# Kernel tuning notes

Hardware: AMD Instinct MI355X
Metric: run time of the kernel (lower is better)

The kernel has to match this reference:

```python
import jax, jax.numpy as jnp
import numpy as np

EPS = 1e-06
N, K, O = 100000, 64, 1024


def setup_inputs() -> dict:
    key = jax.random.key(0)
    k1, k2, k3 = jax.random.split(key, 3)
    # counts: non-negative read counts per particle (scaled uniform, like count data)
    counts = jnp.floor(jax.random.uniform(k1, (N, O), dtype=jnp.float32) * 10.0)
    # otu_dist: K community profiles over O OTUs (simplex rows)
    otu_raw = jax.random.uniform(k2, (K, O), dtype=jnp.float32) + 1e-3
    otu_dist = otu_raw / otu_raw.sum(axis=-1, keepdims=True)
    # comm_dist: mixture weights over K communities (simplex)
    comm_raw = jax.random.uniform(k3, (K,), dtype=jnp.float32) + 1e-3
    comm_dist = comm_raw / comm_raw.sum()
    return {"counts": counts, "otu_dist": otu_dist, "comm_dist": comm_dist}


def reference(counts, otu_dist, comm_dist):
    # (counts[:,None,:] * log(otu_dist[None,:,:]+EPS)).sum(-1) == counts @ log(otu_dist+EPS).T
    # (N,K) per-particle per-community log-likelihood + log prior weight
    log_otu = jnp.log(otu_dist + EPS)                      # (K, O)
    logsumexpand = jnp.einsum('no,ko->nk', counts, log_otu) + jnp.log(comm_dist + EPS)[None, :]
    summand = jax.scipy.special.logsumexp(logsumexpand, axis=1)  # (N,)
    return summand.sum()
```

## Files before the change

kernel.cpp:

```cpp
#include <hip/hip_runtime.h>
#include <hip/hip_bf16.h>
#include <math.h>

#define NP 100000
#define KC 64
#define OD 1024
#define EPSF 1e-6f

#define ROWS_PER_BLOCK 128
#define NBLOCKS ((NP + ROWS_PER_BLOCK - 1) / ROWS_PER_BLOCK)

typedef __attribute__((ext_vector_type(8))) short short8;
typedef __attribute__((ext_vector_type(4))) float f32x4;

#define WS_LOGW      0
#define WS_PARTIALS  256
#define WS_BHI       8192
#define WS_BLO       (8192 + KC * OD * 2)

__device__ __forceinline__ unsigned short f32_bf16_rn(float f) {
  unsigned int u = __float_as_uint(f);
  unsigned int r = u + 0x7fffu + ((u >> 16) & 1u);
  return (unsigned short)(r >> 16);
}

__global__ void prep_kernel(const float* __restrict__ otu,
                            const float* __restrict__ comm,
                            unsigned short* __restrict__ bhi,
                            unsigned short* __restrict__ blo,
                            float* __restrict__ logw) {
  int b = blockIdx.x;
  if (b < KC) {
    const float* src = otu + b * OD;
    for (int o = threadIdx.x; o < OD; o += blockDim.x) {
      float x = logf(src[o] + EPSF);
      unsigned short h = f32_bf16_rn(x);
      float hf = __uint_as_float(((unsigned int)h) << 16);
      unsigned short l = f32_bf16_rn(x - hf);
      bhi[b * OD + o] = h;
      blo[b * OD + o] = l;
    }
  } else {
    if (threadIdx.x < KC) logw[threadIdx.x] = logf(comm[threadIdx.x] + EPSF);
  }
}

__global__ __launch_bounds__(256, 3)
void ll_kernel(const float* __restrict__ counts,
               const unsigned short* __restrict__ bhi,
               const unsigned short* __restrict__ blo,
               const float* __restrict__ logw,
               double* __restrict__ partials) {
  const int tid = threadIdx.x;
  const int wave = tid >> 6;
  const int lane = tid & 63;
  const int g = lane >> 4;
  const int c = lane & 15;
  const int rowBase = blockIdx.x * ROWS_PER_BLOCK + wave * 32;

  f32x4 acc[2][4];
#pragma unroll
  for (int i = 0; i < 2; ++i)
#pragma unroll
    for (int j = 0; j < 4; ++j)
      acc[i][j] = (f32x4){0.f, 0.f, 0.f, 0.f};

  int r0 = rowBase + c;      if (r0 >= NP) r0 = NP - 1;
  int r1 = rowBase + 16 + c; if (r1 >= NP) r1 = NP - 1;
  const float* pa0 = counts + (size_t)r0 * OD + g * 8;
  const float* pa1 = counts + (size_t)r1 * OD + g * 8;
  const unsigned short* pbh = bhi + (size_t)c * OD + g * 8;
  const unsigned short* pbl = blo + (size_t)c * OD + g * 8;

  for (int ko = 0; ko < OD; ko += 32) {
    float4 a0lo = *(const float4*)(pa0 + ko);
    float4 a0hi = *(const float4*)(pa0 + ko + 4);
    float4 a1lo = *(const float4*)(pa1 + ko);
    float4 a1hi = *(const float4*)(pa1 + ko + 4);

    short8 fbh[4], fbl[4];
#pragma unroll
    for (int ct = 0; ct < 4; ++ct) {
      fbh[ct] = *(const short8*)(pbh + (size_t)(ct * 16) * OD + ko);
      fbl[ct] = *(const short8*)(pbl + (size_t)(ct * 16) * OD + ko);
    }

    union { unsigned int u[4]; short8 v; } ua0, ua1;
    ua0.u[0] = __builtin_amdgcn_perm(__float_as_uint(a0lo.y), __float_as_uint(a0lo.x), 0x07060302u);
    ua0.u[1] = __builtin_amdgcn_perm(__float_as_uint(a0lo.w), __float_as_uint(a0lo.z), 0x07060302u);
    ua0.u[2] = __builtin_amdgcn_perm(__float_as_uint(a0hi.y), __float_as_uint(a0hi.x), 0x07060302u);
    ua0.u[3] = __builtin_amdgcn_perm(__float_as_uint(a0hi.w), __float_as_uint(a0hi.z), 0x07060302u);
    ua1.u[0] = __builtin_amdgcn_perm(__float_as_uint(a1lo.y), __float_as_uint(a1lo.x), 0x07060302u);
    ua1.u[1] = __builtin_amdgcn_perm(__float_as_uint(a1lo.w), __float_as_uint(a1lo.z), 0x07060302u);
    ua1.u[2] = __builtin_amdgcn_perm(__float_as_uint(a1hi.y), __float_as_uint(a1hi.x), 0x07060302u);
    ua1.u[3] = __builtin_amdgcn_perm(__float_as_uint(a1hi.w), __float_as_uint(a1hi.z), 0x07060302u);

#pragma unroll
    for (int ct = 0; ct < 4; ++ct) {
      acc[0][ct] = __builtin_amdgcn_mfma_f32_16x16x32_bf16(ua0.v, fbh[ct], acc[0][ct], 0, 0, 0);
      acc[1][ct] = __builtin_amdgcn_mfma_f32_16x16x32_bf16(ua1.v, fbh[ct], acc[1][ct], 0, 0, 0);
      acc[0][ct] = __builtin_amdgcn_mfma_f32_16x16x32_bf16(ua0.v, fbl[ct], acc[0][ct], 0, 0, 0);
      acc[1][ct] = __builtin_amdgcn_mfma_f32_16x16x32_bf16(ua1.v, fbl[ct], acc[1][ct], 0, 0, 0);
    }
  }

  float lw[4];
#pragma unroll
  for (int ct = 0; ct < 4; ++ct) lw[ct] = logw[ct * 16 + c];

  double lsum = 0.0;
#pragma unroll
  for (int rt = 0; rt < 2; ++rt) {
#pragma unroll
    for (int r = 0; r < 4; ++r) {
      float v0 = acc[rt][0][r] + lw[0];
      float v1 = acc[rt][1][r] + lw[1];
      float v2 = acc[rt][2][r] + lw[2];
      float v3 = acc[rt][3][r] + lw[3];
      float m = fmaxf(fmaxf(v0, v1), fmaxf(v2, v3));
      m = fmaxf(m, __shfl_xor(m, 1));
      m = fmaxf(m, __shfl_xor(m, 2));
      m = fmaxf(m, __shfl_xor(m, 4));
      m = fmaxf(m, __shfl_xor(m, 8));
      float s = __expf(v0 - m) + __expf(v1 - m) + __expf(v2 - m) + __expf(v3 - m);
      s += __shfl_xor(s, 1);
      s += __shfl_xor(s, 2);
      s += __shfl_xor(s, 4);
      s += __shfl_xor(s, 8);
      float lse = m + __logf(s);
      int row = rowBase + rt * 16 + g * 4 + r;
      if (c == 0 && row < NP) lsum += (double)lse;
    }
  }
  lsum += __shfl_xor(lsum, 16);
  lsum += __shfl_xor(lsum, 32);

  __shared__ double wpart[4];
  if (lane == 0) wpart[wave] = lsum;
  __syncthreads();
  if (tid == 0) partials[blockIdx.x] = wpart[0] + wpart[1] + wpart[2] + wpart[3];
}

__global__ void finalize_kernel(const double* __restrict__ partials,
                                float* __restrict__ out) {
  double s = 0.0;
  for (int i = threadIdx.x; i < NBLOCKS; i += 256) s += partials[i];
  s += __shfl_xor(s, 1);
  s += __shfl_xor(s, 2);
  s += __shfl_xor(s, 4);
  s += __shfl_xor(s, 8);
  s += __shfl_xor(s, 16);
  s += __shfl_xor(s, 32);
  __shared__ double sp[4];
  int w = threadIdx.x >> 6, lane = threadIdx.x & 63;
  if (lane == 0) sp[w] = s;
  __syncthreads();
  if (threadIdx.x == 0) out[0] = (float)(sp[0] + sp[1] + sp[2] + sp[3]);
}

extern "C" void kernel_launch(void* const* d_in, const int* in_sizes, int n_in,
                              void* d_out, int out_size, void* d_ws, size_t ws_size,
                              hipStream_t stream) {
  const float* counts = (const float*)d_in[0];
  const float* otu    = (const float*)d_in[1];
  const float* comm   = (const float*)d_in[2];
  float* out = (float*)d_out;
  char* ws = (char*)d_ws;

  float* logw            = (float*)(ws + WS_LOGW);
  double* partials       = (double*)(ws + WS_PARTIALS);
  unsigned short* bhi    = (unsigned short*)(ws + WS_BHI);
  unsigned short* blo    = (unsigned short*)(ws + WS_BLO);

  prep_kernel<<<KC + 1, 256, 0, stream>>>(otu, comm, bhi, blo, logw);
  ll_kernel<<<NBLOCKS, 256, 0, stream>>>(counts, bhi, blo, logw, partials);
  finalize_kernel<<<1, 256, 0, stream>>>(partials, out);
}
```

Measured before the change: 616.8 us.

## Stage B fragments in LDS with double-buffered async global-to-LDS loads

The prep kernel now writes the split bf16 log-OTU matrix in a pre-swizzled per-k-tile layout matching the MFMA fragment order. The main kernel loads each k-tile of B into a double-buffered shared-memory buffer using global_load_lds, shared by all four waves. It also prefetches the next counts tile into registers while computing the current one. Previously each wave fetched its B fragments from global memory on its own. This cuts redundant global/L2 traffic and overlaps loads with MFMA work, at the cost of a block barrier every k-step and extra LDS use that may lower occupancy.

```diff
diff --git a/kernel.cpp b/kernel.cpp
--- a/kernel.cpp
+++ b/kernel.cpp
@@ -9,14 +9,14 @@
 
 #define ROWS_PER_BLOCK 128
 #define NBLOCKS ((NP + ROWS_PER_BLOCK - 1) / ROWS_PER_BLOCK)
+#define NT 32
 
 typedef __attribute__((ext_vector_type(8))) short short8;
 typedef __attribute__((ext_vector_type(4))) float f32x4;
 
 #define WS_LOGW      0
 #define WS_PARTIALS  256
-#define WS_BHI       8192
-#define WS_BLO       (8192 + KC * OD * 2)
+#define WS_BSTAGE    8192
 
 __device__ __forceinline__ unsigned short f32_bf16_rn(float f) {
   unsigned int u = __float_as_uint(f);
@@ -24,21 +24,28 @@
   return (unsigned short)(r >> 16);
 }
 
+__device__ __forceinline__ void gll16(const void* gsrc, void* lds) {
+  __builtin_amdgcn_global_load_lds(
+      (const __attribute__((address_space(1))) unsigned int*)gsrc,
+      (__attribute__((address_space(3))) unsigned int*)lds, 16, 0, 0);
+}
+
 __global__ void prep_kernel(const float* __restrict__ otu,
                             const float* __restrict__ comm,
-                            unsigned short* __restrict__ bhi,
-                            unsigned short* __restrict__ blo,
+                            unsigned short* __restrict__ bstage,
                             float* __restrict__ logw) {
   int b = blockIdx.x;
   if (b < KC) {
-    const float* src = otu + b * OD;
-    for (int o = threadIdx.x; o < OD; o += blockDim.x) {
-      float x = logf(src[o] + EPSF);
+    int c = b & 15, ct = b >> 4;
+    for (int k = threadIdx.x; k < OD; k += blockDim.x) {
+      float x = logf(otu[b * OD + k] + EPSF);
       unsigned short h = f32_bf16_rn(x);
       float hf = __uint_as_float(((unsigned int)h) << 16);
       unsigned short l = f32_bf16_rn(x - hf);
-      bhi[b * OD + o] = h;
-      blo[b * OD + o] = l;
+      int t = k >> 5, g = (k >> 3) & 3, kk = k & 7;
+      size_t base = (size_t)t * 4096 + (size_t)ct * 512 + (size_t)(g * 16 + c) * 8 + kk;
+      bstage[base] = h;
+      bstage[base + 2048] = l;
     }
   } else {
     if (threadIdx.x < KC) logw[threadIdx.x] = logf(comm[threadIdx.x] + EPSF);
@@ -47,10 +54,11 @@
 
 __global__ __launch_bounds__(256, 3)
 void ll_kernel(const float* __restrict__ counts,
-               const unsigned short* __restrict__ bhi,
-               const unsigned short* __restrict__ blo,
+               const unsigned short* __restrict__ bstage,
                const float* __restrict__ logw,
                double* __restrict__ partials) {
+  __shared__ unsigned short bufB[2][4096];
+
   const int tid = threadIdx.x;
   const int wave = tid >> 6;
   const int lane = tid & 63;
@@ -69,20 +77,42 @@
   int r1 = rowBase + 16 + c; if (r1 >= NP) r1 = NP - 1;
   const float* pa0 = counts + (size_t)r0 * OD + g * 8;
   const float* pa1 = counts + (size_t)r1 * OD + g * 8;
-  const unsigned short* pbh = bhi + (size_t)c * OD + g * 8;
-  const unsigned short* pbl = blo + (size_t)c * OD + g * 8;
-
-  for (int ko = 0; ko < OD; ko += 32) {
-    float4 a0lo = *(const float4*)(pa0 + ko);
-    float4 a0hi = *(const float4*)(pa0 + ko + 4);
-    float4 a1lo = *(const float4*)(pa1 + ko);
-    float4 a1hi = *(const float4*)(pa1 + ko + 4);
-
+
+  const unsigned short* sbase = bstage + (size_t)wave * 1024 + (size_t)lane * 8;
+  unsigned short* dbase0 = &bufB[0][wave * 1024];
+  unsigned short* dbase1 = &bufB[1][wave * 1024];
+
+  gll16(sbase, dbase0);
+  gll16(sbase + 512, dbase0 + 512);
+  float4 a0lo = *(const float4*)(pa0);
+  float4 a0hi = *(const float4*)(pa0 + 4);
+  float4 a1lo = *(const float4*)(pa1);
+  float4 a1hi = *(const float4*)(pa1 + 4);
+  asm volatile("s_waitcnt vmcnt(0)" ::: "memory");
+  __syncthreads();
+
+  int cur = 0;
+  for (int t = 0; t < NT; ++t) {
+    const int tn = (t + 1 < NT) ? t + 1 : NT - 1;
+
+    const unsigned short* src = sbase + (size_t)tn * 4096;
+    unsigned short* dst = (cur == 0) ? dbase1 : dbase0;
+    gll16(src, dst);
+    gll16(src + 512, dst + 512);
+    asm volatile("" ::: "memory");
+
+    const int kon = tn * 32;
+    float4 n0lo = *(const float4*)(pa0 + kon);
+    float4 n0hi = *(const float4*)(pa0 + kon + 4);
+    float4 n1lo = *(const float4*)(pa1 + kon);
+    float4 n1hi = *(const float4*)(pa1 + kon + 4);
+
+    const unsigned short* bb = &bufB[cur][0];
     short8 fbh[4], fbl[4];
 #pragma unroll
     for (int ct = 0; ct < 4; ++ct) {
-      fbh[ct] = *(const short8*)(pbh + (size_t)(ct * 16) * OD + ko);
-      fbl[ct] = *(const short8*)(pbl + (size_t)(ct * 16) * OD + ko);
+      fbh[ct] = *(const short8*)(bb + ct * 512 + lane * 8);
+      fbl[ct] = *(const short8*)(bb + 2048 + ct * 512 + lane * 8);
     }
 
     union { unsigned int u[4]; short8 v; } ua0, ua1;
@@ -102,6 +132,12 @@
       acc[0][ct] = __builtin_amdgcn_mfma_f32_16x16x32_bf16(ua0.v, fbl[ct], acc[0][ct], 0, 0, 0);
       acc[1][ct] = __builtin_amdgcn_mfma_f32_16x16x32_bf16(ua1.v, fbl[ct], acc[1][ct], 0, 0, 0);
     }
+
+    asm volatile("s_waitcnt vmcnt(4)" ::: "memory");
+    __builtin_amdgcn_s_barrier();
+
+    a0lo = n0lo; a0hi = n0hi; a1lo = n1lo; a1hi = n1hi;
+    cur ^= 1;
   }
 
   float lw[4];
@@ -167,12 +203,11 @@
   float* out = (float*)d_out;
   char* ws = (char*)d_ws;
 
-  float* logw            = (float*)(ws + WS_LOGW);
-  double* partials       = (double*)(ws + WS_PARTIALS);
-  unsigned short* bhi    = (unsigned short*)(ws + WS_BHI);
-  unsigned short* blo    = (unsigned short*)(ws + WS_BLO);
-
-  prep_kernel<<<KC + 1, 256, 0, stream>>>(otu, comm, bhi, blo, logw);
-  ll_kernel<<<NBLOCKS, 256, 0, stream>>>(counts, bhi, blo, logw, partials);
+  float* logw          = (float*)(ws + WS_LOGW);
+  double* partials     = (double*)(ws + WS_PARTIALS);
+  unsigned short* bst  = (unsigned short*)(ws + WS_BSTAGE);
+
+  prep_kernel<<<KC + 1, 256, 0, stream>>>(otu, comm, bst, logw);
+  ll_kernel<<<NBLOCKS, 256, 0, stream>>>(counts, bst, logw, partials);
   finalize_kernel<<<1, 256, 0, stream>>>(partials, out);
 }
```

Result: faster. 571.8 us (-7.3%).
